# Performance work log

Hardware: AMD Instinct MI355X
Metric: run time of the kernel (lower is better)

The kernel has to match this reference:

```python
import jax, jax.numpy as jnp
import numpy as np

D_MODEL = 1024
NUM_HEADS = 16
HEAD_DIM = D_MODEL // NUM_HEADS  # used only for score scaling, as in the torch code


def setup_inputs() -> dict:
    key = jax.random.key(0)
    ks = jax.random.split(key, 8)
    B, S, D = 4, 2048, D_MODEL
    w_scale = 1.0 / np.sqrt(D)
    return {
        "x": jax.random.normal(ks[0], (B, S, D), dtype=jnp.float32),
        "Wq": jax.random.normal(ks[1], (D, D), dtype=jnp.float32) * w_scale,
        "bq": jnp.zeros((D,), dtype=jnp.float32),
        "Wk": jax.random.normal(ks[2], (D, D), dtype=jnp.float32) * w_scale,
        "bk": jnp.zeros((D,), dtype=jnp.float32),
        "Wv": jax.random.normal(ks[3], (D, D), dtype=jnp.float32) * w_scale,
        "bv": jnp.zeros((D,), dtype=jnp.float32),
        "temperature_scale": jnp.ones((1,), dtype=jnp.float32),
    }


def reference(x, Wq, bq, Wk, bk, Wv, bv, temperature_scale):
    # q, k, v: (B, S, D) -- no head split in the original module
    q = x @ Wq + bq
    k = x @ Wk + bk
    v = x @ Wv + bv
    scale = jnp.asarray(HEAD_DIM, x.dtype) ** 0.5
    # scores: (B, S, S)
    scores = jnp.einsum("bqd,bkd->bqk", q, k) / scale / temperature_scale[0]
    probs = jax.nn.softmax(scores, axis=-1)
    # per-row attention entropy (B, S, 1)
    entropy = -jnp.sum(probs * jnp.log(probs + 1e-8), axis=-1, keepdims=True)
    attention_output = jnp.einsum("bqk,bkd->bqd", probs, v)
    return attention_output, entropy.mean()
```

## Files before the change

### kernel.cpp

```cpp
#include <hip/hip_runtime.h>
#include <hip/hip_bf16.h>
#include <cstdint>
#include <cstddef>


typedef __attribute__((ext_vector_type(8))) short short8;
typedef __attribute__((ext_vector_type(4))) short short4v;
typedef __attribute__((ext_vector_type(4))) float f32x4;

#define GLOBAL_AS __attribute__((address_space(1)))
#define LDS_AS __attribute__((address_space(3)))

#define PHASE_BARRIER()                                   \
  do {                                                    \
    __builtin_amdgcn_sched_barrier(0);                    \
    asm volatile("s_barrier" ::: "memory");               \
    __builtin_amdgcn_sched_barrier(0);                    \
  } while (0)

__device__ __forceinline__ void async_load16(const void* g, void* lds) {
  __builtin_amdgcn_global_load_lds((GLOBAL_AS void*)g, (LDS_AS void*)lds, 16, 0, 0);
}

__device__ __forceinline__ short f2bf_s(float x) {
  __hip_bfloat16 h = __float2bfloat16(x);
  return *reinterpret_cast<short*>(&h);
}

template <int MODE>
__device__ __forceinline__
void gemm256_body(const __hip_bfloat16* __restrict__ A,
                  const __hip_bfloat16* __restrict__ Bt,
                  void* __restrict__ Cout,
                  const float* __restrict__ bias,
                  int K, int lda, int ldb, int ldc,
                  __hip_bfloat16* __restrict__ sA,
                  __hip_bfloat16* __restrict__ sB,
                  int m0, int n0,
                  const float* __restrict__ aux,
                  float* __restrict__ stats) {
  const int tid  = threadIdx.x;
  const int lane = tid & 63;
  const int wid  = tid >> 6;
  const int wm   = (wid >> 2) * 128;
  const int wn   = (wid & 3) * 64;
  const int quad = lane >> 4;
  const int rc   = lane & 15;
  const int rc7  = rc & 7;
  const int wnr  = wn & 64;

  f32x4 acc[8][4] = {};

  const int r0   = tid >> 3;
  const int scol = ((tid & 7) ^ (r0 & 7)) * 8;
  const __hip_bfloat16* Ag = A  + (size_t)(m0 + r0) * lda + scol;
  const __hip_bfloat16* Bg = Bt + (size_t)(n0 + r0) * ldb + scol;

  const int NT = K >> 6;

  auto stA = [&](int buf, int half, int kofs) {
    const __hip_bfloat16* s = Ag + (size_t)(half * 128) * lda + kofs;
    __hip_bfloat16* d = sA + (size_t)buf * 16384 + (size_t)half * 8192 + tid * 8;
    async_load16(s, d);
    async_load16(s + (size_t)64 * lda, d + 4096);
  };
  auto stB = [&](int buf, int half, int kofs) {
    const __hip_bfloat16* s = Bg + (size_t)(half * 128) * ldb + kofs;
    __hip_bfloat16* d = sB + (size_t)buf * 16384 + (size_t)half * 8192 + tid * 8;
    async_load16(s, d);
    async_load16(s + (size_t)64 * ldb, d + 4096);
  };

  const __hip_bfloat16* sAh = sA + (size_t)(wm >> 7) * 8192;
  const __hip_bfloat16* sBh = sB + (size_t)(wn >> 7) * 8192;

  short8 af[2][4], ah[2][4], blo[2][2], bhi[2][2];

  {
    const int k1 = (NT > 1) ? 64 : 0;
    stA(0, 0, 0);  stA(0, 1, 0);  stB(0, 0, 0);  stB(0, 1, 0);
    stA(1, 0, k1); stA(1, 1, k1); stB(1, 0, k1); stB(1, 1, k1);
  }
  asm volatile("s_waitcnt vmcnt(8)" ::: "memory");
  PHASE_BARRIER();
#pragma unroll
  for (int kk = 0; kk < 2; ++kk) {
    const int gs = ((kk * 4 + quad) ^ rc7) * 8;
#pragma unroll
    for (int i = 0; i < 4; ++i)
      af[kk][i] = *(const short8*)&sAh[(i * 16 + rc) * 64 + gs];
#pragma unroll
    for (int j = 0; j < 2; ++j)
      blo[kk][j] = *(const short8*)&sBh[(wnr + j * 16 + rc) * 64 + gs];
  }

  for (int t = 0; t < NT; ++t) {
    const int buf = t & 1;
    const __hip_bfloat16* sAc = sAh + buf * 16384;
    const __hip_bfloat16* sBc = sBh + buf * 16384;
    const __hip_bfloat16* sAn = sAh + (buf ^ 1) * 16384;
    const __hip_bfloat16* sBn = sBh + (buf ^ 1) * 16384;
    const int k2 = ((t + 2 < NT) ? t + 2 : NT - 1) * 64;

#pragma unroll
    for (int kk = 0; kk < 2; ++kk) {
      const int gs = ((kk * 4 + quad) ^ rc7) * 8;
#pragma unroll
      for (int i = 0; i < 4; ++i)
        ah[kk][i] = *(const short8*)&sAc[((i + 4) * 16 + rc) * 64 + gs];
    }
    PHASE_BARRIER();
    __builtin_amdgcn_s_setprio(1);
#pragma unroll
    for (int mi = 0; mi < 4; ++mi)
#pragma unroll
      for (int ni = 0; ni < 2; ++ni)
#pragma unroll
        for (int kk = 0; kk < 2; ++kk)
          acc[mi][ni] = __builtin_amdgcn_mfma_f32_16x16x32_bf16(
              af[kk][mi], blo[kk][ni], acc[mi][ni], 0, 0, 0);
    __builtin_amdgcn_s_setprio(0);
    PHASE_BARRIER();

#pragma unroll
    for (int kk = 0; kk < 2; ++kk) {
      const int gs = ((kk * 4 + quad) ^ rc7) * 8;
#pragma unroll
      for (int j = 0; j < 2; ++j)
        bhi[kk][j] = *(const short8*)&sBc[(wnr + (j + 2) * 16 + rc) * 64 + gs];
    }
    PHASE_BARRIER();
    __builtin_amdgcn_s_setprio(1);
#pragma unroll
    for (int mi = 0; mi < 4; ++mi)
#pragma unroll
      for (int ni = 0; ni < 2; ++ni)
#pragma unroll
        for (int kk = 0; kk < 2; ++kk)
          acc[4 + mi][ni] = __builtin_amdgcn_mfma_f32_16x16x32_bf16(
              ah[kk][mi], blo[kk][ni], acc[4 + mi][ni], 0, 0, 0);
    __builtin_amdgcn_s_setprio(0);
    asm volatile("s_waitcnt vmcnt(0)" ::: "memory");
    PHASE_BARRIER();

    stA(buf, 1, k2);
    stB(buf, 0, k2);
#pragma unroll
    for (int kk = 0; kk < 2; ++kk) {
      const int gs = ((kk * 4 + quad) ^ rc7) * 8;
#pragma unroll
      for (int j = 0; j < 2; ++j)
        blo[kk][j] = *(const short8*)&sBn[(wnr + j * 16 + rc) * 64 + gs];
    }
    PHASE_BARRIER();
    __builtin_amdgcn_s_setprio(1);
#pragma unroll
    for (int mi = 0; mi < 4; ++mi)
#pragma unroll
      for (int nj = 0; nj < 2; ++nj)
#pragma unroll
        for (int kk = 0; kk < 2; ++kk)
          acc[mi][2 + nj] = __builtin_amdgcn_mfma_f32_16x16x32_bf16(
              af[kk][mi], bhi[kk][nj], acc[mi][2 + nj], 0, 0, 0);
    __builtin_amdgcn_s_setprio(0);
    PHASE_BARRIER();

    stA(buf, 0, k2);
    stB(buf, 1, k2);
#pragma unroll
    for (int kk = 0; kk < 2; ++kk) {
      const int gs = ((kk * 4 + quad) ^ rc7) * 8;
#pragma unroll
      for (int i = 0; i < 4; ++i)
        af[kk][i] = *(const short8*)&sAn[(i * 16 + rc) * 64 + gs];
    }
    PHASE_BARRIER();
    __builtin_amdgcn_s_setprio(1);
#pragma unroll
    for (int mi = 0; mi < 4; ++mi)
#pragma unroll
      for (int nj = 0; nj < 2; ++nj)
#pragma unroll
        for (int kk = 0; kk < 2; ++kk)
          acc[4 + mi][2 + nj] = __builtin_amdgcn_mfma_f32_16x16x32_bf16(
              ah[kk][mi], bhi[kk][nj], acc[4 + mi][2 + nj], 0, 0, 0);
    __builtin_amdgcn_s_setprio(0);
    PHASE_BARRIER();
  }
  asm volatile("s_waitcnt vmcnt(0)" ::: "memory");

  if (MODE == 3) {
    const int chunk = (n0 + wn) >> 6;
#pragma unroll
    for (int mi = 0; mi < 8; ++mi) {
      float l_acc[4] = {}, w_acc[4] = {};
#pragma unroll
      for (int ni = 0; ni < 4; ++ni)
#pragma unroll
        for (int r = 0; r < 4; ++r) {
          const float xv = acc[mi][ni][r];
          const float e = __expf(xv);
          acc[mi][ni][r] = e;
          l_acc[r] += e;
          w_acc[r] += e * xv;
        }
#pragma unroll
      for (int r = 0; r < 4; ++r) {
        float l = l_acc[r], w = w_acc[r];
#pragma unroll
        for (int off = 1; off < 16; off <<= 1) {
          l += __shfl_xor(l, off);
          w += __shfl_xor(w, off);
        }
        if (rc == 0) {
          const int row = m0 + wm + mi * 16 + quad * 4 + r;
          *(float2*)&stats[((size_t)row * 32 + chunk) * 2] = make_float2(l, w);
        }
      }
#pragma unroll
      for (int ni = 0; ni < 4; ++ni) {
        const int col = n0 + wn + ni * 16 + rc;
#pragma unroll
        for (int r = 0; r < 4; ++r) {
          const int row = m0 + wm + mi * 16 + quad * 4 + r;
          ((__hip_bfloat16*)Cout)[(size_t)row * ldc + col] =
              __float2bfloat16(acc[mi][ni][r]);
        }
      }
    }
  } else {
    const float qsc = (MODE == 1 && aux) ? 1.0f / (8.0f * aux[0]) : 1.0f;
#pragma unroll
    for (int mi = 0; mi < 8; ++mi) {
#pragma unroll
      for (int ni = 0; ni < 4; ++ni) {
        const int col = n0 + wn + ni * 16 + rc;
        const float badd = bias[col];
        if (MODE == 2) {
          const int rowb = m0 + wm + mi * 16 + quad * 4;
          short4v o;
#pragma unroll
          for (int r = 0; r < 4; ++r) o[r] = f2bf_s(acc[mi][ni][r] + badd);
          const size_t idx = (size_t)(rowb >> 11) * (1024u * 2048u) +
                             (size_t)col * 2048u + (size_t)(rowb & 2047);
          *(short4v*)((short*)Cout + idx) = o;
        } else {
#pragma unroll
          for (int r = 0; r < 4; ++r) {
            const int row = m0 + wm + mi * 16 + quad * 4 + r;
            ((__hip_bfloat16*)Cout)[(size_t)row * ldc + col] =
                __float2bfloat16((acc[mi][ni][r] + badd) * qsc);
          }
        }
      }
    }
  }
}

__global__ __launch_bounds__(512, 2)
void qkv_fused256(const __hip_bfloat16* __restrict__ xb,
                  const __hip_bfloat16* __restrict__ Wt,
                  __hip_bfloat16* __restrict__ qb, __hip_bfloat16* __restrict__ kb,
                  __hip_bfloat16* __restrict__ vt,
                  const float* __restrict__ bq, const float* __restrict__ bk,
                  const float* __restrict__ bv, const float* __restrict__ tptr) {
  extern __shared__ __align__(16) __hip_bfloat16 smem[];
  __hip_bfloat16* sA = smem;
  __hip_bfloat16* sB = smem + 32768;
  const int lin = blockIdx.x;
  const int G  = (lin & 7) * 48 + (lin >> 3);
  const int mt = G / 12, nt = G % 12;
  const int m0  = mt * 256;
  const int n0g = nt * 256;
  const int z   = n0g >> 10;
  const int n0  = n0g & 1023;
  const __hip_bfloat16* B = Wt + (size_t)z * 1024 * 1024;
  if (z == 0)
    gemm256_body<1>(xb, B, qb, bq, 1024, 1024, 1024, 1024, sA, sB, m0, n0, tptr, nullptr);
  else if (z == 1)
    gemm256_body<1>(xb, B, kb, bk, 1024, 1024, 1024, 1024, sA, sB, m0, n0, nullptr, nullptr);
  else
    gemm256_body<2>(xb, B, vt, bv, 1024, 1024, 1024, 0, sA, sB, m0, n0, nullptr, nullptr);
}

__global__ __launch_bounds__(512, 2)
void scores256(const __hip_bfloat16* __restrict__ qb,
               const __hip_bfloat16* __restrict__ kb,
               __hip_bfloat16* __restrict__ Pt,
               float* __restrict__ stats) {
  extern __shared__ __align__(16) __hip_bfloat16 smem[];
  __hip_bfloat16* sA = smem;
  __hip_bfloat16* sB = smem + 32768;
  const int lin = blockIdx.x;
  const int G = (lin & 7) * 32 + (lin >> 3);
  const int z = G >> 6;
  const int r = G & 63;
  const int y = r >> 3, x = r & 7;
  gemm256_body<3>(qb + (size_t)z * 2048 * 1024, kb + (size_t)z * 2048 * 1024,
                  Pt + (size_t)z * 2048 * 2048, nullptr, 1024, 1024, 1024, 2048,
                  sA, sB, y * 256, x * 256, nullptr, stats + (size_t)z * 2048 * 64);
}

template <int MODE>
__device__ __forceinline__
void gemm_body(const __hip_bfloat16* __restrict__ A,
               const __hip_bfloat16* __restrict__ Bt,
               void* __restrict__ Cout,
               const float* __restrict__ bias,
               int K, int lda, int ldb, int ldc,
               __hip_bfloat16* __restrict__ sA,
               __hip_bfloat16* __restrict__ sB,
               int m0, int n0,
               const float* __restrict__ aux,
               float* __restrict__ stats) {
  const int tid  = threadIdx.x;
  const int lane = tid & 63;
  const int wid  = tid >> 6;
  const int wm = (wid >> 1) * 64;
  const int wn = (wid & 1) * 64;
  const int quad = lane >> 4;
  const int rc   = lane & 15;

  f32x4 acc[4][4] = {};

  const int srow = tid >> 3;
  const int scol = ((tid & 7) ^ ((tid >> 3) & 7)) * 8;
  const __hip_bfloat16* Ag = A  + (size_t)(m0 + srow) * lda + scol;
  const __hip_bfloat16* Bg = Bt + (size_t)(n0 + srow) * ldb + scol;

  for (int k0 = 0; k0 < K; k0 += 64) {
#pragma unroll
    for (int p = 0; p < 4; ++p) {
      async_load16(Ag + k0 + (size_t)(32 * p) * lda, &sA[(wid * 64 + 256 * p) * 8]);
      async_load16(Bg + k0 + (size_t)(32 * p) * ldb, &sB[(wid * 64 + 256 * p) * 8]);
    }
    __syncthreads();

#pragma unroll
    for (int kk = 0; kk < 2; ++kk) {
      const int xo = ((kk * 4 + quad) ^ (rc & 7)) * 8;
      short8 af[4], bf[4];
#pragma unroll
      for (int i = 0; i < 4; ++i)
        af[i] = *(const short8*)&sA[(wm + i * 16 + rc) * 64 + xo];
#pragma unroll
      for (int i = 0; i < 4; ++i)
        bf[i] = *(const short8*)&sB[(wn + i * 16 + rc) * 64 + xo];

#pragma unroll
      for (int mi = 0; mi < 4; ++mi)
#pragma unroll
        for (int ni = 0; ni < 4; ++ni)
          acc[mi][ni] = __builtin_amdgcn_mfma_f32_16x16x32_bf16(
              af[mi], bf[ni], acc[mi][ni], 0, 0, 0);
    }
    __syncthreads();
  }

  if (MODE == 4) {
#pragma unroll
    for (int mi = 0; mi < 4; ++mi) {
      float sc[4];
#pragma unroll
      for (int r = 0; r < 4; ++r)
        sc[r] = aux[m0 + wm + mi * 16 + quad * 4 + r];
#pragma unroll
      for (int ni = 0; ni < 4; ++ni) {
        const int col = n0 + wn + ni * 16 + rc;
#pragma unroll
        for (int r = 0; r < 4; ++r) {
          const int row = m0 + wm + mi * 16 + quad * 4 + r;
          ((float*)Cout)[(size_t)row * ldc + col] = acc[mi][ni][r] * sc[r];
        }
      }
    }
  }
}

__global__ __launch_bounds__(256)
void pv_swz(const __hip_bfloat16* __restrict__ Pt,
            const __hip_bfloat16* __restrict__ vt,
            float* __restrict__ out,
            const float* __restrict__ inv_l) {
  __shared__ __align__(16) __hip_bfloat16 sA[128 * 64];
  __shared__ __align__(16) __hip_bfloat16 sB[128 * 64];
  const int lin = blockIdx.x;
  const int j = lin & 7, t = lin >> 3;
  const int w = t & 3;
  const int G = j + 8 * (t >> 2);
  const size_t z = G >> 5;
  const int r = G & 31;
  const int y = (r >> 2) * 2 + (w >> 1);
  const int x = (r & 3) * 2 + (w & 1);
  gemm_body<4>(Pt + z * 2048 * 2048, vt + z * 1024 * 2048,
               out + z * 2048 * 1024, nullptr, 2048, 2048, 2048, 1024,
               sA, sB, y * 128, x * 128, inv_l + z * 2048, nullptr);
}

__global__ __launch_bounds__(256)
void prep_fused(const float* __restrict__ x, __hip_bfloat16* __restrict__ xb,
                const float* __restrict__ Wq, const float* __restrict__ Wk,
                const float* __restrict__ Wv, __hip_bfloat16* __restrict__ Wt) {
  if (blockIdx.x < 4096) {
    const int i = (blockIdx.x * 256 + threadIdx.x) * 8;
    const float4 a = *(const float4*)(x + i);
    const float4 b = *(const float4*)(x + i + 4);
    short8 o;
    o[0] = f2bf_s(a.x); o[1] = f2bf_s(a.y); o[2] = f2bf_s(a.z); o[3] = f2bf_s(a.w);
    o[4] = f2bf_s(b.x); o[5] = f2bf_s(b.y); o[6] = f2bf_s(b.z); o[7] = f2bf_s(b.w);
    *(short8*)((short*)xb + i) = o;
  } else {
    __shared__ float tile[64][65];
    const int b = blockIdx.x - 4096;
    const int z = b >> 8;
    const int rem = b & 255;
    const int c0 = (rem & 15) * 64;
    const int r0 = (rem >> 4) * 64;
    const float* src = (z == 0) ? Wq : (z == 1) ? Wk : Wv;
    __hip_bfloat16* dst = Wt + (size_t)z * 1024 * 1024;
    const int lane = threadIdx.x & 63;
    const int grp  = threadIdx.x >> 6;
#pragma unroll
    for (int i = 0; i < 16; ++i) {
      const int r = grp * 16 + i;
      tile[r][lane] = src[(size_t)(r0 + r) * 1024 + c0 + lane];
    }
    __syncthreads();
#pragma unroll
    for (int i = 0; i < 16; ++i) {
      const int r = grp * 16 + i;
      dst[(size_t)(c0 + r) * 1024 + r0 + lane] = __float2bfloat16(tile[lane][r]);
    }
  }
}

__global__ __launch_bounds__(256)
void stats_reduce(const float* __restrict__ stats,
                  float* __restrict__ inv_l, float* __restrict__ Hrow) {
  const int row = blockIdx.x * 256 + threadIdx.x;
  const float* sp = stats + (size_t)row * 64;
  float l = 0.f, w = 0.f;
#pragma unroll
  for (int j = 0; j < 16; ++j) {
    const float4 a = *(const float4*)(sp + j * 4);
    l += a.x + a.z;
    w += a.y + a.w;
  }
  const float il = 1.0f / l;
  inv_l[row] = il;
  Hrow[row] = __logf(l) - w * il;
}

__global__ __launch_bounds__(256)
void reduce_entropy(const float* __restrict__ Hrow, float* __restrict__ out) {
  const int tid  = threadIdx.x;
  const int lane = tid & 63;
  const int wid  = tid >> 6;
  float s = 0.f;
#pragma unroll
  for (int j = 0; j < 8; ++j) {
    const float4 a = *(const float4*)(Hrow + j * 1024 + tid * 4);
    s += a.x + a.y + a.z + a.w;
  }
#pragma unroll
  for (int off = 1; off < 64; off <<= 1) s += __shfl_xor(s, off);
  __shared__ float red[4];
  if (lane == 0) red[wid] = s;
  __syncthreads();
  if (tid == 0)
    out[0] = (red[0] + red[1] + red[2] + red[3]) * (1.0f / 8192.0f);
}

extern "C" void kernel_launch(void* const* d_in, const int* in_sizes, int n_in,
                              void* d_out, int out_size, void* d_ws, size_t ws_size,
                              hipStream_t stream) {
  const float* x    = (const float*)d_in[0];
  const float* Wq   = (const float*)d_in[1];
  const float* bq   = (const float*)d_in[2];
  const float* Wk   = (const float*)d_in[3];
  const float* bk   = (const float*)d_in[4];
  const float* Wv   = (const float*)d_in[5];
  const float* bv   = (const float*)d_in[6];
  const float* temp = (const float*)d_in[7];
  float* out = (float*)d_out;
  char* ws = (char*)d_ws;

  __hip_bfloat16* qb    = (__hip_bfloat16*)(ws + 0);
  __hip_bfloat16* kb    = (__hip_bfloat16*)(ws + 16777216);
  __hip_bfloat16* vt    = (__hip_bfloat16*)(ws + 33554432);
  __hip_bfloat16* xb    = (__hip_bfloat16*)(ws + 50331648);
  __hip_bfloat16* Wt    = (__hip_bfloat16*)(ws + 67108864);
  __hip_bfloat16* Pt    = (__hip_bfloat16*)(ws + 73400320);
  float*          stats = (float*)(ws + 106954752);
  float*          inv_l = (float*)(ws + 109051904);
  float*          Hrow  = (float*)(ws + 109084672);

  static bool attr_done = false;
  if (!attr_done) {
    hipFuncSetAttribute((const void*)qkv_fused256,
                        hipFuncAttributeMaxDynamicSharedMemorySize, 131072);
    hipFuncSetAttribute((const void*)scores256,
                        hipFuncAttributeMaxDynamicSharedMemorySize, 131072);
    attr_done = true;
  }

  prep_fused<<<4864, 256, 0, stream>>>(x, xb, Wq, Wk, Wv, Wt);

  qkv_fused256<<<384, 512, 131072, stream>>>(xb, Wt, qb, kb, vt, bq, bk, bv, temp);

  scores256<<<256, 512, 131072, stream>>>(qb, kb, Pt, stats);
  stats_reduce<<<32, 256, 0, stream>>>(stats, inv_l, Hrow);
  pv_swz<<<512, 256, 0, stream>>>(Pt, vt, out, inv_l);

  reduce_entropy<<<1, 256, 0, stream>>>(Hrow, out + 8388608);
}
```

Measured before the change: 261.7 us.

## Reschedule 256-tile GEMM prefetches and fold stats reduction into PV epilogue

The 256-tile GEMM main loop now issues the next-stage A and B global-to-LDS loads earlier, spread across the MFMA phases, and waits on vmcnt(4) instead of draining all loads. It also adds explicit lgkmcnt waits before the barriers. Separately, the stats_reduce kernel is removed and each PV block recomputes row sums, inverse normaliser and per-row entropy from the stats buffer in its epilogue, saving one launch and a round-trip through inv_l. The cost is redundant stats reads across column blocks and an extra block barrier, and the earlier LDS overwrite depends on the barrier ordering being correct.

```diff
diff --git a/kernel.cpp b/kernel.cpp
--- a/kernel.cpp
+++ b/kernel.cpp
@@ -15,6 +15,12 @@
   do {                                                    \
     __builtin_amdgcn_sched_barrier(0);                    \
     asm volatile("s_barrier" ::: "memory");               \
+    __builtin_amdgcn_sched_barrier(0);                    \
+  } while (0)
+
+#define LGKM0()                                           \
+  do {                                                    \
+    asm volatile("s_waitcnt lgkmcnt(0)" ::: "memory");    \
     __builtin_amdgcn_sched_barrier(0);                    \
   } while (0)
 
@@ -93,6 +99,7 @@
     for (int j = 0; j < 2; ++j)
       blo[kk][j] = *(const short8*)&sBh[(wnr + j * 16 + rc) * 64 + gs];
   }
+  LGKM0();
 
   for (int t = 0; t < NT; ++t) {
     const int buf = t & 1;
@@ -109,6 +116,7 @@
       for (int i = 0; i < 4; ++i)
         ah[kk][i] = *(const short8*)&sAc[((i + 4) * 16 + rc) * 64 + gs];
     }
+    LGKM0();
     PHASE_BARRIER();
     __builtin_amdgcn_s_setprio(1);
 #pragma unroll
@@ -129,6 +137,9 @@
       for (int j = 0; j < 2; ++j)
         bhi[kk][j] = *(const short8*)&sBc[(wnr + (j + 2) * 16 + rc) * 64 + gs];
     }
+    stA(buf, 0, k2);
+    stA(buf, 1, k2);
+    LGKM0();
     PHASE_BARRIER();
     __builtin_amdgcn_s_setprio(1);
 #pragma unroll
@@ -140,11 +151,9 @@
           acc[4 + mi][ni] = __builtin_amdgcn_mfma_f32_16x16x32_bf16(
               ah[kk][mi], blo[kk][ni], acc[4 + mi][ni], 0, 0, 0);
     __builtin_amdgcn_s_setprio(0);
-    asm volatile("s_waitcnt vmcnt(0)" ::: "memory");
-    PHASE_BARRIER();
-
-    stA(buf, 1, k2);
-    stB(buf, 0, k2);
+    asm volatile("s_waitcnt vmcnt(4)" ::: "memory");
+    PHASE_BARRIER();
+
 #pragma unroll
     for (int kk = 0; kk < 2; ++kk) {
       const int gs = ((kk * 4 + quad) ^ rc7) * 8;
@@ -152,6 +161,9 @@
       for (int j = 0; j < 2; ++j)
         blo[kk][j] = *(const short8*)&sBn[(wnr + j * 16 + rc) * 64 + gs];
     }
+    stB(buf, 0, k2);
+    stB(buf, 1, k2);
+    LGKM0();
     PHASE_BARRIER();
     __builtin_amdgcn_s_setprio(1);
 #pragma unroll
@@ -165,8 +177,6 @@
     __builtin_amdgcn_s_setprio(0);
     PHASE_BARRIER();
 
-    stA(buf, 0, k2);
-    stB(buf, 1, k2);
 #pragma unroll
     for (int kk = 0; kk < 2; ++kk) {
       const int gs = ((kk * 4 + quad) ^ rc7) * 8;
@@ -174,6 +184,7 @@
       for (int i = 0; i < 4; ++i)
         af[kk][i] = *(const short8*)&sAn[(i * 16 + rc) * 64 + gs];
     }
+    LGKM0();
     PHASE_BARRIER();
     __builtin_amdgcn_s_setprio(1);
 #pragma unroll
@@ -301,18 +312,16 @@
                   sA, sB, y * 256, x * 256, nullptr, stats + (size_t)z * 2048 * 64);
 }
 
-template <int MODE>
 __device__ __forceinline__
-void gemm_body(const __hip_bfloat16* __restrict__ A,
-               const __hip_bfloat16* __restrict__ Bt,
-               void* __restrict__ Cout,
-               const float* __restrict__ bias,
-               int K, int lda, int ldb, int ldc,
-               __hip_bfloat16* __restrict__ sA,
-               __hip_bfloat16* __restrict__ sB,
-               int m0, int n0,
-               const float* __restrict__ aux,
-               float* __restrict__ stats) {
+void gemm_pv(const __hip_bfloat16* __restrict__ A,
+             const __hip_bfloat16* __restrict__ Bt,
+             float* __restrict__ Cout,
+             int K, int lda, int ldb, int ldc,
+             __hip_bfloat16* __restrict__ sA,
+             __hip_bfloat16* __restrict__ sB,
+             int m0, int n0,
+             const float* __restrict__ aux,
+             float* __restrict__ Hrow) {
   const int tid  = threadIdx.x;
   const int lane = tid & 63;
   const int wid  = tid >> 6;
@@ -357,21 +366,38 @@
     __syncthreads();
   }
 
-  if (MODE == 4) {
-#pragma unroll
-    for (int mi = 0; mi < 4; ++mi) {
-      float sc[4];
-#pragma unroll
-      for (int r = 0; r < 4; ++r)
-        sc[r] = aux[m0 + wm + mi * 16 + quad * 4 + r];
-#pragma unroll
-      for (int ni = 0; ni < 4; ++ni) {
-        const int col = n0 + wn + ni * 16 + rc;
-#pragma unroll
-        for (int r = 0; r < 4; ++r) {
-          const int row = m0 + wm + mi * 16 + quad * 4 + r;
-          ((float*)Cout)[(size_t)row * ldc + col] = acc[mi][ni][r] * sc[r];
-        }
+  float* lred = (float*)sA;
+  {
+    const int row2 = tid >> 1;
+    const float* sp = aux + (size_t)(m0 + row2) * 64 + (tid & 1) * 32;
+    float l = 0.f, w = 0.f;
+#pragma unroll
+    for (int j = 0; j < 8; ++j) {
+      const float4 a = *(const float4*)(sp + j * 4);
+      l += a.x + a.z;
+      w += a.y + a.w;
+    }
+    l += __shfl_xor(l, 1);
+    w += __shfl_xor(w, 1);
+    if ((tid & 1) == 0) {
+      lred[row2] = 1.0f / l;
+      if (Hrow) Hrow[m0 + row2] = __logf(l) - w / l;
+    }
+  }
+  __syncthreads();
+#pragma unroll
+  for (int mi = 0; mi < 4; ++mi) {
+    float sc[4];
+#pragma unroll
+    for (int r = 0; r < 4; ++r)
+      sc[r] = lred[wm + mi * 16 + quad * 4 + r];
+#pragma unroll
+    for (int ni = 0; ni < 4; ++ni) {
+      const int col = n0 + wn + ni * 16 + rc;
+#pragma unroll
+      for (int r = 0; r < 4; ++r) {
+        const int row = m0 + wm + mi * 16 + quad * 4 + r;
+        Cout[(size_t)row * ldc + col] = acc[mi][ni][r] * sc[r];
       }
     }
   }
@@ -381,7 +407,8 @@
 void pv_swz(const __hip_bfloat16* __restrict__ Pt,
             const __hip_bfloat16* __restrict__ vt,
             float* __restrict__ out,
-            const float* __restrict__ inv_l) {
+            const float* __restrict__ stats,
+            float* __restrict__ Hrow) {
   __shared__ __align__(16) __hip_bfloat16 sA[128 * 64];
   __shared__ __align__(16) __hip_bfloat16 sB[128 * 64];
   const int lin = blockIdx.x;
@@ -392,9 +419,11 @@
   const int r = G & 31;
   const int y = (r >> 2) * 2 + (w >> 1);
   const int x = (r & 3) * 2 + (w & 1);
-  gemm_body<4>(Pt + z * 2048 * 2048, vt + z * 1024 * 2048,
-               out + z * 2048 * 1024, nullptr, 2048, 2048, 2048, 1024,
-               sA, sB, y * 128, x * 128, inv_l + z * 2048, nullptr);
+  gemm_pv(Pt + z * 2048 * 2048, vt + z * 1024 * 2048,
+          out + z * 2048 * 1024, 2048, 2048, 2048, 1024,
+          sA, sB, y * 128, x * 128,
+          stats + z * 2048 * 64,
+          (x == 0) ? (Hrow + z * 2048) : nullptr);
 }
 
 __global__ __launch_bounds__(256)
@@ -435,23 +464,6 @@
 }
 
 __global__ __launch_bounds__(256)
-void stats_reduce(const float* __restrict__ stats,
-                  float* __restrict__ inv_l, float* __restrict__ Hrow) {
-  const int row = blockIdx.x * 256 + threadIdx.x;
-  const float* sp = stats + (size_t)row * 64;
-  float l = 0.f, w = 0.f;
-#pragma unroll
-  for (int j = 0; j < 16; ++j) {
-    const float4 a = *(const float4*)(sp + j * 4);
-    l += a.x + a.z;
-    w += a.y + a.w;
-  }
-  const float il = 1.0f / l;
-  inv_l[row] = il;
-  Hrow[row] = __logf(l) - w * il;
-}
-
-__global__ __launch_bounds__(256)
 void reduce_entropy(const float* __restrict__ Hrow, float* __restrict__ out) {
   const int tid  = threadIdx.x;
   const int lane = tid & 63;
@@ -492,7 +504,6 @@
   __hip_bfloat16* Wt    = (__hip_bfloat16*)(ws + 67108864);
   __hip_bfloat16* Pt    = (__hip_bfloat16*)(ws + 73400320);
   float*          stats = (float*)(ws + 106954752);
-  float*          inv_l = (float*)(ws + 109051904);
   float*          Hrow  = (float*)(ws + 109084672);
 
   static bool attr_done = false;
@@ -509,8 +520,7 @@
   qkv_fused256<<<384, 512, 131072, stream>>>(xb, Wt, qb, kb, vt, bq, bk, bv, temp);
 
   scores256<<<256, 512, 131072, stream>>>(qb, kb, Pt, stats);
-  stats_reduce<<<32, 256, 0, stream>>>(stats, inv_l, Hrow);
-  pv_swz<<<512, 256, 0, stream>>>(Pt, vt, out, inv_l);
+  pv_swz<<<512, 256, 0, stream>>>(Pt, vt, out, stats, Hrow);
 
   reduce_entropy<<<1, 256, 0, stream>>>(Hrow, out + 8388608);
 }
```

Result: no change. 262.2 us (+0.2%).
